# Kernel optimization log

Measured on AMD Instinct MI355X. Metric: run time of the kernel, lower is better.

The kernel has to match this reference:

```python
import jax, jax.numpy as jnp
import numpy as np

B, C_IN, C_OUT, T, N, KS = 16, 64, 64, 48, 1024, 3

def setup_inputs() -> dict:
    key = jax.random.key(0)
    k1, k2, k3, k4 = jax.random.split(key, 4)
    x = jax.random.normal(k1, (B, C_IN, T, N), dtype=jnp.float32)
    Lk = jax.random.normal(k2, (KS, N, N), dtype=jnp.float32) / np.sqrt(N)
    # kaiming-uniform-like init for theta, uniform for b
    fan_in = C_IN * KS
    bound_t = np.sqrt(6.0 / fan_in)
    theta = jax.random.uniform(k3, (C_IN, C_OUT, KS), dtype=jnp.float32,
                               minval=-bound_t, maxval=bound_t)
    bound_b = 1.0 / np.sqrt(fan_in)
    b = jax.random.uniform(k4, (1, C_OUT, 1, 1), dtype=jnp.float32,
                           minval=-bound_b, maxval=bound_b)
    return {"x": x, "Lk": Lk, "theta": theta, "b": b}

def reference(x, Lk, theta, b):
    # x: [B, c_in, T, N], Lk: [ks, N, N], theta: [c_in, c_out, ks], b: [1, c_out, 1, 1]
    x_c = jnp.einsum('knm,bitm->bitkn', Lk, x)          # [B, c_in, T, ks, N]
    x_gc = jnp.einsum('iok,bitkn->botn', theta, x_c) + b  # [B, c_out, T, N]
    # Align: c_in == c_out -> identity
    return jax.nn.relu(x_gc + x)
```

## Files before the change

### kernel.cpp

```cpp
#include <hip/hip_runtime.h>
#include <hip/hip_bf16.h>
#include <stdint.h>


typedef short bs8 __attribute__((ext_vector_type(8)));
typedef float f32x4 __attribute__((ext_vector_type(4)));

#define NB   16
#define NC   64
#define NT   48
#define NN   1024
#define NKS  3
#define KDIM 3072
#define KT   48

__device__ __forceinline__ short f2bs(float f) {
  uint32_t u = __builtin_bit_cast(uint32_t, f);
  u = (u + 0x7FFFu + ((u >> 16) & 1u)) >> 16;
  return (short)u;
}

__device__ __forceinline__ void gload16(const void* g, void* l) {
  __builtin_amdgcn_global_load_lds(
      (const __attribute__((address_space(1))) void*)g,
      (__attribute__((address_space(3))) void*)l, 16, 0, 0);
}

__global__ __launch_bounds__(256) void k_prep_bt(const float* __restrict__ Lk,
                                                 short* __restrict__ BT) {
  int gid = blockIdx.x * 256 + threadIdx.x;
  int e = gid * 4;
  int k = e >> 20;
  int rem = e & 1048575;
  int n = rem >> 10;
  int m = rem & 1023;
  float4 v = *reinterpret_cast<const float4*>(Lk + e);
  union { short s[4]; uint64_t u; } p;
  p.s[0] = f2bs(v.x); p.s[1] = f2bs(v.y); p.s[2] = f2bs(v.z); p.s[3] = f2bs(v.w);
  *reinterpret_cast<uint64_t*>(BT + (size_t)n * KDIM + k * NN + m) = p.u;
}

__global__ __launch_bounds__(256) void k_step1(const float* __restrict__ x,
                                               const float* __restrict__ theta,
                                               short* __restrict__ Y, int b0) {
  __shared__ __align__(16) short th[NKS * 64 * 72];
  int tid = threadIdx.x;
  for (int idx = tid; idx < NC * NC * NKS; idx += 256) {
    int i = idx / (NC * NKS);
    int r = idx - i * (NC * NKS);
    int o = r / NKS;
    int k = r - o * NKS;
    th[(k * 64 + o) * 72 + i] = f2bs(theta[idx]);
  }
  __syncthreads();

  int bid = blockIdx.x;
  int mt  = bid & 3;
  int btl = bid >> 2;
  int b_l = btl / NT;
  int t   = btl - b_l * NT;
  int b   = b0 + b_l;

  int lane = tid & 63, wave = tid >> 6;
  int l15 = lane & 15, lg = lane >> 4;
  const float* xb = x + (size_t)b * (NC * NT * NN) + (size_t)t * NN;
  int m0 = mt * 256 + wave * 64;
  size_t yrow0 = (size_t)btl * 64;

  for (int ni = 0; ni < 4; ++ni) {
    int mcol = m0 + ni * 16 + l15;
    float xv[16];
#pragma unroll
    for (int j = 0; j < 16; ++j) {
      int i = ((j >> 3) << 5) + lg * 8 + (j & 7);
      xv[j] = xb[(size_t)i * (NT * NN) + mcol];
    }
    f32x4 acc[3][4];
#pragma unroll
    for (int k = 0; k < 3; ++k)
#pragma unroll
      for (int mi = 0; mi < 4; ++mi)
        acc[k][mi] = (f32x4){0.f, 0.f, 0.f, 0.f};

#pragma unroll
    for (int ks = 0; ks < 2; ++ks) {
      bs8 bfrag;
#pragma unroll
      for (int j = 0; j < 8; ++j) bfrag[j] = f2bs(xv[ks * 8 + j]);
#pragma unroll
      for (int mi = 0; mi < 4; ++mi) {
#pragma unroll
        for (int k = 0; k < 3; ++k) {
          const bs8* ap = reinterpret_cast<const bs8*>(
              &th[(k * 64 + mi * 16 + l15) * 72 + ks * 32 + lg * 8]);
          acc[k][mi] = __builtin_amdgcn_mfma_f32_16x16x32_bf16(
              *ap, bfrag, acc[k][mi], 0, 0, 0);
        }
      }
    }
#pragma unroll
    for (int k = 0; k < 3; ++k)
#pragma unroll
      for (int mi = 0; mi < 4; ++mi)
#pragma unroll
        for (int q = 0; q < 4; ++q) {
          int o = mi * 16 + lg * 4 + q;
          Y[(yrow0 + o) * KDIM + k * NN + mcol] = f2bs(acc[k][mi][q]);
        }
  }
}


__device__ __forceinline__ void stage_half(const short* __restrict__ src,
                                           short* lds, int h, int tid) {
  int wave = tid >> 6;
#pragma unroll
  for (int r = 0; r < 2; ++r) {
    int idx = h * 1024 + r * 512 + tid;
    int row = idx >> 3, c8 = idx & 7;
    int c8s = c8 ^ (row & 7);
    gload16(src + (size_t)row * KDIM + c8s * 8,
            lds + (h * 1024 + r * 512 + wave * 64) * 8);
  }
}

#define BARRIER()                              \
  __builtin_amdgcn_sched_barrier(0);           \
  __builtin_amdgcn_s_barrier();                \
  __builtin_amdgcn_sched_barrier(0);

#define READ_A(QM)                                                        \
  _Pragma("unroll") for (int e = 0; e < 4; ++e)                           \
    _Pragma("unroll") for (int ks = 0; ks < 2; ++ks) {                    \
      int rw = (8 * (QM) + 2 * e + wr) * 16 + l15;                        \
      af[e][ks] = *(const bs8*)&AL[p * 16384 + rw * 64 +                  \
                    ((ks * 32 + lg * 8) ^ ((rw & 7) << 3))];              \
    }

#define READ_B(BF, QN)                                                    \
  _Pragma("unroll") for (int f = 0; f < 2; ++f)                           \
    _Pragma("unroll") for (int ks = 0; ks < 2; ++ks) {                    \
      int rw = (8 * (QN) + 4 * f + wc) * 16 + l15;                        \
      BF[f][ks] = *(const bs8*)&BL[p * 16384 + rw * 64 +                  \
                    ((ks * 32 + lg * 8) ^ ((rw & 7) << 3))];              \
    }

#define COMPUTE(QM, BF, QN)                                                 \
  __builtin_amdgcn_s_setprio(1);                                            \
  _Pragma("unroll") for (int ks = 0; ks < 2; ++ks)                          \
    _Pragma("unroll") for (int e = 0; e < 4; ++e)                           \
      _Pragma("unroll") for (int f = 0; f < 2; ++f)                         \
        acc[4 * (QM) + e][2 * (QN) + f] =                                   \
            __builtin_amdgcn_mfma_f32_16x16x32_bf16(                        \
                af[e][ks], BF[f][ks], acc[4 * (QM) + e][2 * (QN) + f],      \
                0, 0, 0);                                                   \
  __builtin_amdgcn_s_setprio(0);

__global__ __launch_bounds__(512, 2) void k_gemm(const short* __restrict__ Y,
                                                 const short* __restrict__ BT,
                                                 const float* __restrict__ x,
                                                 const float* __restrict__ bias,
                                                 float* __restrict__ out,
                                                 int b0, int nwg) {
  __shared__ __align__(16) short AL[2 * 16384];
  __shared__ __align__(16) short BL[2 * 16384];

  int bid = blockIdx.x;
  int cpx = nwg >> 3;
  int swz = (bid & 7) * cpx + (bid >> 3);
  int colb = swz & 3;
  int rowb = swz >> 2;

  int tid = threadIdx.x;
  int lane = tid & 63, wave = tid >> 6;
  int wr = wave >> 2, wc = wave & 3;
  int l15 = lane & 15, lg = lane >> 4;
  int row0 = rowb * 256, col0 = colb * 256;

  const short* Yb  = Y  + (size_t)row0 * KDIM;
  const short* BTb = BT + (size_t)col0 * KDIM;

  f32x4 acc[8][4];
#pragma unroll
  for (int j = 0; j < 8; ++j)
#pragma unroll
    for (int i = 0; i < 4; ++i) acc[j][i] = (f32x4){0.f, 0.f, 0.f, 0.f};

  stage_half(Yb,        AL,         0, tid);
  stage_half(Yb,        AL,         1, tid);
  stage_half(BTb,       BL,         0, tid);
  stage_half(BTb,       BL,         1, tid);
  stage_half(Yb + 64,   AL + 16384, 0, tid);
  stage_half(BTb + 64,  BL + 16384, 0, tid);
  asm volatile("s_waitcnt vmcnt(4)" ::: "memory");
  BARRIER();

#pragma unroll 2
  for (int t = 0; t < KT; ++t) {
    int p = t & 1;
    const short* Y1 = Yb + (t + 1) * 64;
    const short* B1 = BTb + (t + 1) * 64;
    const short* Y2 = Yb + (t + 2) * 64;
    const short* B2 = BTb + (t + 2) * 64;
    bs8 af[4][2], bf0[2][2], bf1[2][2];

    READ_A(0)
    READ_B(bf0, 0)
    if (t < KT - 1) stage_half(Y1, AL + (p ^ 1) * 16384, 1, tid);
    BARRIER();
    COMPUTE(0, bf0, 0)
    BARRIER();

    READ_B(bf1, 1)
    if (t < KT - 1) stage_half(B1, BL + (p ^ 1) * 16384, 1, tid);
    BARRIER();
    COMPUTE(0, bf1, 1)
    BARRIER();

    READ_A(1)
    if (t < KT - 2) stage_half(Y2, AL + p * 16384, 0, tid);
    BARRIER();
    COMPUTE(1, bf1, 1)
    BARRIER();

    if (t < KT - 2) stage_half(B2, BL + p * 16384, 0, tid);
    BARRIER();
    COMPUTE(1, bf0, 0)
    if (t < KT - 2) { asm volatile("s_waitcnt vmcnt(4)" ::: "memory"); }
    else            { asm volatile("s_waitcnt vmcnt(0)" ::: "memory"); }
    BARRIER();
  }

#pragma unroll
  for (int j = 0; j < 8; ++j) {
#pragma unroll
    for (int q = 0; q < 4; ++q) {
      int r = row0 + (2 * j + wr) * 16 + lg * 4 + q;
      int o = r & 63;
      int btl = r >> 6;
      int tt = btl % NT;
      int bb = b0 + btl / NT;
      float bo = bias[o];
      size_t obase = ((size_t)(bb * 64 + o) * NT + tt) * NN;
#pragma unroll
      for (int i = 0; i < 4; ++i) {
        int n = col0 + (4 * i + wc) * 16 + l15;
        size_t oidx = obase + n;
        float v = acc[j][i][q] + bo + x[oidx];
        out[oidx] = v > 0.f ? v : 0.f;
      }
    }
  }
}

extern "C" void kernel_launch(void* const* d_in, const int* in_sizes, int n_in,
                              void* d_out, int out_size, void* d_ws, size_t ws_size,
                              hipStream_t stream) {
  const float* x     = (const float*)d_in[0];
  const float* Lk    = (const float*)d_in[1];
  const float* theta = (const float*)d_in[2];
  const float* bias  = (const float*)d_in[3];
  float* out = (float*)d_out;

  char* ws = (char*)d_ws;
  short* BT = (short*)ws;
  short* Y  = (short*)(ws + (size_t)(8u << 20));
  size_t avail = ws_size > ((size_t)8u << 20) ? ws_size - ((size_t)8u << 20) : 0;
  size_t perB = (size_t)NT * NC * KDIM * 2;
  int bc = 16;
  while (bc > 1 && (size_t)bc * perB > avail) bc >>= 1;

  k_prep_bt<<<dim3(3072), dim3(256), 0, stream>>>(Lk, BT);
  for (int b0 = 0; b0 < NB; b0 += bc) {
    k_step1<<<dim3(bc * 192), dim3(256), 0, stream>>>(x, theta, Y, b0);
    int nwg = bc * 48;
    k_gemm<<<dim3(nwg), dim3(512), 0, stream>>>(Y, BT, x, bias, out, b0, nwg);
  }
}
```

Before: 571.8 us.

## Software-pipeline LDS fragment reads across GEMM k-tiles with fewer barriers

Restructures the GEMM main loop so LDS fragment reads for the next sub-block, including the first A/B fragments of the next k-tile, are issued before the MFMA block that precedes them. This halves the barriers per k-tile (from eight to four) and uses per-phase vmcnt waits instead of a single wait at the end of the tile. Ping-pong fragment registers (afX/afY, bf0a/bf0b) and explicit peeled final tiles replace the generic loop. The extra live fragment registers raise register pressure, which could hurt at two workgroups per CU, and the cross-stage LDS reuse relies on the barrier ordering being correct.

```diff
diff --git a/kernel.cpp b/kernel.cpp
--- a/kernel.cpp
+++ b/kernel.cpp
@@ -124,37 +124,60 @@
   }
 }
 
-#define BARRIER()                              \
-  __builtin_amdgcn_sched_barrier(0);           \
+#define VMC(N) asm volatile("s_waitcnt vmcnt(" #N ")" ::: "memory")
+#define BARR()                                 \
   __builtin_amdgcn_s_barrier();                \
   __builtin_amdgcn_sched_barrier(0);
 
-#define READ_A(QM)                                                        \
+#define READ_A(DST, QM, P)                                                \
   _Pragma("unroll") for (int e = 0; e < 4; ++e)                           \
     _Pragma("unroll") for (int ks = 0; ks < 2; ++ks) {                    \
       int rw = (8 * (QM) + 2 * e + wr) * 16 + l15;                        \
-      af[e][ks] = *(const bs8*)&AL[p * 16384 + rw * 64 +                  \
+      DST[e][ks] = *(const bs8*)&AL[(P) * 16384 + rw * 64 +               \
                     ((ks * 32 + lg * 8) ^ ((rw & 7) << 3))];              \
     }
 
-#define READ_B(BF, QN)                                                    \
+#define READ_B(DST, QN, P)                                                \
   _Pragma("unroll") for (int f = 0; f < 2; ++f)                           \
     _Pragma("unroll") for (int ks = 0; ks < 2; ++ks) {                    \
       int rw = (8 * (QN) + 4 * f + wc) * 16 + l15;                        \
-      BF[f][ks] = *(const bs8*)&BL[p * 16384 + rw * 64 +                  \
+      DST[f][ks] = *(const bs8*)&BL[(P) * 16384 + rw * 64 +               \
                     ((ks * 32 + lg * 8) ^ ((rw & 7) << 3))];              \
     }
 
-#define COMPUTE(QM, BF, QN)                                                 \
+#define COMPUTE(QM, AF, BF, QN)                                             \
   __builtin_amdgcn_s_setprio(1);                                            \
   _Pragma("unroll") for (int ks = 0; ks < 2; ++ks)                          \
     _Pragma("unroll") for (int e = 0; e < 4; ++e)                           \
       _Pragma("unroll") for (int f = 0; f < 2; ++f)                         \
         acc[4 * (QM) + e][2 * (QN) + f] =                                   \
             __builtin_amdgcn_mfma_f32_16x16x32_bf16(                        \
-                af[e][ks], BF[f][ks], acc[4 * (QM) + e][2 * (QN) + f],      \
+                AF[e][ks], BF[f][ks], acc[4 * (QM) + e][2 * (QN) + f],      \
                 0, 0, 0);                                                   \
   __builtin_amdgcn_s_setprio(0);
+
+#define TILE(t, P, B0C, B0N, S1, S2, V1, V2, V3)                            \
+  {                                                                         \
+    READ_B(bfq, 1, P);                                                      \
+    if (S1) stage_half(Yb + ((t) + 1) * 64, AL + ((P) ^ 1) * 16384, 1, tid);\
+    BARR();                                                                 \
+    COMPUTE(0, afX, B0C, 0);                                                \
+    READ_A(afY, 1, P);                                                      \
+    if (S1) stage_half(BTb + ((t) + 1) * 64, BL + ((P) ^ 1) * 16384, 1, tid);\
+    V1;                                                                     \
+    BARR();                                                                 \
+    COMPUTE(0, afX, bfq, 1);                                                \
+    if (S1) READ_A(afX, 0, (P) ^ 1);                                        \
+    if (S2) stage_half(Yb + ((t) + 2) * 64, AL + (P) * 16384, 0, tid);      \
+    V2;                                                                     \
+    BARR();                                                                 \
+    COMPUTE(1, afY, bfq, 1);                                                \
+    if (S1) READ_B(B0N, 0, (P) ^ 1);                                        \
+    if (S2) stage_half(BTb + ((t) + 2) * 64, BL + (P) * 16384, 0, tid);     \
+    V3;                                                                     \
+    BARR();                                                                 \
+    COMPUTE(1, afY, B0C, 0);                                                \
+  }
 
 __global__ __launch_bounds__(512, 2) void k_gemm(const short* __restrict__ Y,
                                                  const short* __restrict__ BT,
@@ -186,50 +209,25 @@
 #pragma unroll
     for (int i = 0; i < 4; ++i) acc[j][i] = (f32x4){0.f, 0.f, 0.f, 0.f};
 
+  bs8 afX[4][2], afY[4][2], bfq[2][2], bf0a[2][2], bf0b[2][2];
+
   stage_half(Yb,        AL,         0, tid);
   stage_half(Yb,        AL,         1, tid);
   stage_half(BTb,       BL,         0, tid);
   stage_half(BTb,       BL,         1, tid);
   stage_half(Yb + 64,   AL + 16384, 0, tid);
   stage_half(BTb + 64,  BL + 16384, 0, tid);
-  asm volatile("s_waitcnt vmcnt(4)" ::: "memory");
-  BARRIER();
-
-#pragma unroll 2
-  for (int t = 0; t < KT; ++t) {
-    int p = t & 1;
-    const short* Y1 = Yb + (t + 1) * 64;
-    const short* B1 = BTb + (t + 1) * 64;
-    const short* Y2 = Yb + (t + 2) * 64;
-    const short* B2 = BTb + (t + 2) * 64;
-    bs8 af[4][2], bf0[2][2], bf1[2][2];
-
-    READ_A(0)
-    READ_B(bf0, 0)
-    if (t < KT - 1) stage_half(Y1, AL + (p ^ 1) * 16384, 1, tid);
-    BARRIER();
-    COMPUTE(0, bf0, 0)
-    BARRIER();
-
-    READ_B(bf1, 1)
-    if (t < KT - 1) stage_half(B1, BL + (p ^ 1) * 16384, 1, tid);
-    BARRIER();
-    COMPUTE(0, bf1, 1)
-    BARRIER();
-
-    READ_A(1)
-    if (t < KT - 2) stage_half(Y2, AL + p * 16384, 0, tid);
-    BARRIER();
-    COMPUTE(1, bf1, 1)
-    BARRIER();
-
-    if (t < KT - 2) stage_half(B2, BL + p * 16384, 0, tid);
-    BARRIER();
-    COMPUTE(1, bf0, 0)
-    if (t < KT - 2) { asm volatile("s_waitcnt vmcnt(4)" ::: "memory"); }
-    else            { asm volatile("s_waitcnt vmcnt(0)" ::: "memory"); }
-    BARRIER();
-  }
+  VMC(4);
+  BARR();
+  READ_A(afX, 0, 0);
+  READ_B(bf0a, 0, 0);
+
+  for (int t = 0; t < KT - 2; t += 2) {
+    TILE(t,     0, bf0a, bf0b, 1, 1, VMC(6), VMC(6), VMC(4));
+    TILE(t + 1, 1, bf0b, bf0a, 1, 1, VMC(6), VMC(6), VMC(4));
+  }
+  TILE(KT - 2, 0, bf0a, bf0b, 1, 0, VMC(6), VMC(4), VMC(0));
+  TILE(KT - 1, 1, bf0b, bf0a, 0, 0, (void)0, (void)0, (void)0);
 
 #pragma unroll
   for (int j = 0; j < 8; ++j) {
```

Result: slower. 729.7 us (+27.6%).
